# Optimization experiments

Hardware: AMD Instinct MI355X
Metric: run time of the kernel (lower is better)

The kernel has to match this reference:

```python
import jax, jax.numpy as jnp
import numpy as np

N_NODES = 100000
N_EDGES = 3200000
D_IN = 128
D_OUT = 128


def setup_inputs() -> dict:
    key = jax.random.key(0)
    k1, k2, k3, k4, k5, k6 = jax.random.split(key, 6)
    x = jax.random.normal(k1, (N_NODES, D_IN), dtype=jnp.float32)
    edge_row = jax.random.randint(k2, (N_EDGES,), 0, N_NODES)  # destination (adj row)
    edge_col = jax.random.randint(k3, (N_EDGES,), 0, N_NODES)  # source (adj col)
    edge_vals = jax.random.uniform(k4, (N_EDGES,), dtype=jnp.float32)
    stdv = 1.0 / np.sqrt(D_OUT)
    weight = jax.random.uniform(k5, (D_IN, D_OUT), dtype=jnp.float32, minval=-stdv, maxval=stdv)
    bias_param = jax.random.uniform(k6, (D_OUT,), dtype=jnp.float32, minval=-stdv, maxval=stdv)
    return {"x": x, "edge_row": edge_row, "edge_col": edge_col,
            "edge_vals": edge_vals, "weight": weight, "bias_param": bias_param}


def reference(x, edge_row, edge_col, edge_vals, weight, bias_param):
    # support = X @ W  : [N, D_OUT]
    support = x @ weight
    # output = spmm(adj, support): out[r] += v * support[c] for each edge (r, c, v)
    messages = edge_vals[:, None] * support[edge_col]  # [E, D_OUT]
    output = jax.ops.segment_sum(messages, edge_row, num_segments=N_NODES)
    return output + bias_param
```

## Files before the change

### kernel.cpp

```cpp
#include <hip/hip_runtime.h>

typedef unsigned int u32;
typedef unsigned long long u64;
typedef unsigned short u16;
typedef unsigned char u8;

#define NN 100000
#define NE 3200000
#define DIM 128
#define RB 256
#define NBK 391
#define BCAP 9216
#define EB 4096

#define OFF_OFFS 0
#define OFF_WB 400064
#define OFF_BCUR 432832
#define OFF_CVP 434432
#define OFF_SH 13234432
#define SCV_BYTES 14417664

typedef __attribute__((ext_vector_type(8))) short bf16x8;
typedef __attribute__((ext_vector_type(4))) float f32x4;

__device__ __forceinline__ float bflo(u32 b) { return __uint_as_float(b << 16); }
__device__ __forceinline__ float bfhi(u32 b) { return __uint_as_float(b & 0xffff0000u); }
__device__ __forceinline__ u16 f2bf(float f) {
    u32 u = __float_as_uint(f);
    return (u16)((u + 0x7fffu + ((u >> 16) & 1u)) >> 16);
}

__global__ __launch_bounds__(256) void bin_kernel(const int4* __restrict__ erow4,
                                                  const int4* __restrict__ ecol4,
                                                  const float4* __restrict__ ev4,
                                                  int* __restrict__ bcur,
                                                  u32* __restrict__ scv,
                                                  u8* __restrict__ slr,
                                                  const float* __restrict__ wf,
                                                  uint4* __restrict__ wB4) {
    __shared__ u32 sscv[EB];
    __shared__ u32 skey[EB];
    __shared__ int sa[512], sb[512], rs[512];
    __shared__ int base[NBK], lcur[NBK];
    int t = threadIdx.x;
    int gid = blockIdx.x * 256 + t;
    if (gid < 2048) {
        int tile = gid >> 6, l = gid & 63;
        int kt = tile >> 3, n = tile & 7;
        int col = n * 16 + (l & 15);
        int kb = kt * 32 + (l >> 4) * 8;
        u32 wp[4];
#pragma unroll
        for (int jj = 0; jj < 4; ++jj) {
            float w0 = wf[(kb + 2 * jj) * DIM + col];
            float w1 = wf[(kb + 2 * jj + 1) * DIM + col];
            wp[jj] = (u32)f2bf(w0) | ((u32)f2bf(w1) << 16);
        }
        wB4[tile * 64 + l] = make_uint4(wp[0], wp[1], wp[2], wp[3]);
    }
    int e0 = blockIdx.x * EB;
    int nval = min(EB, NE - e0);
    int4 er[4];
    bool val[4];
#pragma unroll
    for (int k = 0; k < 4; ++k) {
        int idx4 = (e0 >> 2) + k * 256 + t;
        val[k] = idx4 < NE / 4;
        er[k] = val[k] ? erow4[idx4] : make_int4(0, 0, 0, 0);
    }
    for (int i = t; i < 512; i += 256) sa[i] = 0;
    __syncthreads();
#pragma unroll
    for (int k = 0; k < 4; ++k) {
        if (val[k]) {
            atomicAdd(&sa[er[k].x >> 8], 1);
            atomicAdd(&sa[er[k].y >> 8], 1);
            atomicAdd(&sa[er[k].z >> 8], 1);
            atomicAdd(&sa[er[k].w >> 8], 1);
        }
    }
    __syncthreads();
    for (int i = t; i < NBK; i += 256) base[i] = atomicAdd(&bcur[i], sa[i]);
    int* pa = sa; int* pb = sb;
    for (int d = 1; d < 512; d <<= 1) {
        for (int i = t; i < 512; i += 256)
            pb[i] = (i >= d) ? (pa[i] + pa[i - d]) : pa[i];
        __syncthreads();
        int* tmp = pa; pa = pb; pb = tmp;
    }
    for (int i = t; i < 512; i += 256) {
        int ex = i ? pa[i - 1] : 0;
        rs[i] = ex;
        if (i < NBK) lcur[i] = ex;
    }
    __syncthreads();
#pragma unroll
    for (int k = 0; k < 4; ++k) {
        if (val[k]) {
            int idx4 = (e0 >> 2) + k * 256 + t;
            int4 c = ecol4[idx4];
            float4 v = ev4[idx4];
            int r, b, pos;
            r = er[k].x; b = r >> 8; pos = atomicAdd(&lcur[b], 1);
            sscv[pos] = ((u32)f2bf(v.x) << 17) | (u32)c.x; skey[pos] = ((u32)b << 8) | (u32)(r & 255);
            r = er[k].y; b = r >> 8; pos = atomicAdd(&lcur[b], 1);
            sscv[pos] = ((u32)f2bf(v.y) << 17) | (u32)c.y; skey[pos] = ((u32)b << 8) | (u32)(r & 255);
            r = er[k].z; b = r >> 8; pos = atomicAdd(&lcur[b], 1);
            sscv[pos] = ((u32)f2bf(v.z) << 17) | (u32)c.z; skey[pos] = ((u32)b << 8) | (u32)(r & 255);
            r = er[k].w; b = r >> 8; pos = atomicAdd(&lcur[b], 1);
            sscv[pos] = ((u32)f2bf(v.w) << 17) | (u32)c.w; skey[pos] = ((u32)b << 8) | (u32)(r & 255);
        }
    }
    __syncthreads();
    for (int i = t; i < nval; i += 256) {
        u32 key = skey[i];
        int bk = key >> 8;
        int gl = base[bk] + (i - rs[bk]);
        if (gl < BCAP) {
            scv[bk * BCAP + gl] = sscv[i];
            slr[bk * BCAP + gl] = (u8)(key & 255);
        }
    }
}

__global__ __launch_bounds__(256) void csr_kernel(const u32* __restrict__ scv,
                                                  const u8* __restrict__ slr,
                                                  const int* __restrict__ bcur,
                                                  int* __restrict__ offs,
                                                  u32* __restrict__ cvp) {
    __shared__ u32 lcv[BCAP];
    __shared__ int sa[RB], sb[RB], lcur[RB], red[256];
    int b = blockIdx.x, t = threadIdx.x;
    int r0 = b * RB;
    int rows = min(RB, NN - r0);
    int n = min(bcur[b], BCAP);
    int p = 0;
    for (int i = t; i < b; i += 256) p += min(bcur[i], BCAP);
    red[t] = p;
    sa[t] = 0;
    __syncthreads();
    for (int d = 128; d; d >>= 1) {
        if (t < d) red[t] += red[t + d];
        __syncthreads();
    }
    int gbase = red[0];
    if (b == NBK - 1 && t == 0) offs[NN] = gbase + n;
    const u32* scvB = scv + (size_t)b * BCAP;
    const u8* slrB = slr + (size_t)b * BCAP;
    for (int i = t; i < n; i += 256) atomicAdd(&sa[slrB[i]], 1);
    __syncthreads();
    int* pa = sa; int* pb = sb;
    for (int d = 1; d < 256; d <<= 1) {
        pb[t] = (t >= d) ? (pa[t] + pa[t - d]) : pa[t];
        __syncthreads();
        int* tmp = pa; pa = pb; pb = tmp;
    }
    int excl = t ? pa[t - 1] : 0;
    if (t < rows) offs[r0 + t] = gbase + excl;
    lcur[t] = excl;
    __syncthreads();
    for (int i = t; i < n; i += 256) {
        u32 cv = scvB[i];
        int lr = slrB[i];
        int pos = atomicAdd(&lcur[lr], 1);
        lcv[pos] = cv;
    }
    __syncthreads();
    for (int i = t; i < n; i += 256) cvp[gbase + i] = lcv[i];
}

__global__ __launch_bounds__(256) void gemm_kernel(const float4* __restrict__ xf4,
                                                   const uint4* __restrict__ wB4,
                                                   u32* __restrict__ sup) {
    __shared__ u32 st[64][68];
    int t = threadIdx.x, wave = t >> 6, lane = t & 63;
    int l15 = lane & 15, kg = lane >> 4;
    int row = blockIdx.x * 64 + wave * 16 + l15;
    int rc = min(row, NN - 1);
    f32x4 acc[8];
#pragma unroll
    for (int n = 0; n < 8; ++n) acc[n] = (f32x4){0.f, 0.f, 0.f, 0.f};
#pragma unroll
    for (int kt = 0; kt < 4; ++kt) {
        int k0 = kt * 32 + kg * 8;
        int bidx = (rc * DIM + k0) >> 2;
        float4 xa = xf4[bidx];
        float4 xc = xf4[bidx + 1];
        union { u32 u[4]; bf16x8 v; } A;
        A.u[0] = (u32)f2bf(xa.x) | ((u32)f2bf(xa.y) << 16);
        A.u[1] = (u32)f2bf(xa.z) | ((u32)f2bf(xa.w) << 16);
        A.u[2] = (u32)f2bf(xc.x) | ((u32)f2bf(xc.y) << 16);
        A.u[3] = (u32)f2bf(xc.z) | ((u32)f2bf(xc.w) << 16);
#pragma unroll
        for (int n = 0; n < 8; ++n) {
            union { uint4 u; bf16x8 v; } B;
            B.u = wB4[(kt * 8 + n) * 64 + lane];
            acc[n] = __builtin_amdgcn_mfma_f32_16x16x32_bf16(A.v, B.v, acc[n], 0, 0, 0);
        }
    }
    u16* stp = (u16*)st;
    int rbase = wave * 16 + kg * 4;
#pragma unroll
    for (int n = 0; n < 8; ++n)
#pragma unroll
        for (int i = 0; i < 4; ++i)
            stp[(rbase + i) * 136 + n * 16 + l15] = f2bf(acc[n][i]);
    __syncthreads();
    int r0 = blockIdx.x * 64;
    int rmax = min(64, NN - r0);
    for (int idx = t; idx < 4096; idx += 256) {
        int r = idx >> 6, c = idx & 63;
        if (r < rmax) sup[(r0 + r) * 64 + c] = st[r][c];
    }
}

template <int Q>
__device__ __forceinline__ void gstep(u32 pv, int kk, const u32* __restrict__ sup,
                                      int lane, float& a0, float& a1) {
    u32 ps[Q], xr[Q];
#pragma unroll
    for (int q = 0; q < Q; ++q)
        ps[q] = (u32)__builtin_amdgcn_readlane((int)pv, kk + q);
#pragma unroll
    for (int q = 0; q < Q; ++q)
        xr[q] = __hip_atomic_load(sup + ((ps[q] & 0x1ffffu) << 6) + lane,
                                  __ATOMIC_RELAXED, __HIP_MEMORY_SCOPE_AGENT);
#pragma unroll
    for (int q = 0; q < Q; ++q) {
        float v = bflo(ps[q] >> 17);
        a0 = fmaf(v, bflo(xr[q]), a0);
        a1 = fmaf(v, bfhi(xr[q]), a1);
    }
}

__global__ __launch_bounds__(64) void fused_kernel(const int* __restrict__ offs,
                                                   const u32* __restrict__ cvp,
                                                   const u32* __restrict__ sup,
                                                   const float2* __restrict__ bf2v,
                                                   u64* __restrict__ out) {
    int lane = threadIdx.x;
    int gw = blockIdx.x;
    int start = offs[gw];
    int end = offs[gw + 1];
    int cnt = end - start;
    float2 bp = bf2v[lane];
    float a0 = bp.x, a1 = bp.y;
    for (int j = 0; j < cnt; j += 64) {
        u32 pv = (j + lane < cnt) ? __builtin_nontemporal_load(&cvp[start + j + lane]) : 0u;
        int rem = min(64, cnt - j);
        int kk = 0;
        for (; kk + 32 <= rem; kk += 32) gstep<32>(pv, kk, sup, lane, a0, a1);
        for (; kk < rem; kk += 8) gstep<8>(pv, kk, sup, lane, a0, a1);
    }
    u64 bits = (u64)__float_as_uint(a0) | ((u64)__float_as_uint(a1) << 32);
    __builtin_nontemporal_store(bits, &out[gw * 64 + lane]);
}

extern "C" void kernel_launch(void* const* d_in, const int* in_sizes, int n_in,
                              void* d_out, int out_size, void* d_ws, size_t ws_size,
                              hipStream_t stream) {
    const float* x = (const float*)d_in[0];
    const int* erow = (const int*)d_in[1];
    const int* ecol = (const int*)d_in[2];
    const float* ev = (const float*)d_in[3];
    const float* wf = (const float*)d_in[4];
    const float2* bf2v = (const float2*)d_in[5];

    char* ws = (char*)d_ws;
    int* offs = (int*)(ws + OFF_OFFS);
    uint4* wB4 = (uint4*)(ws + OFF_WB);
    int* bcur = (int*)(ws + OFF_BCUR);
    u32* cvp = (u32*)(ws + OFF_CVP);
    u32* scv = (u32*)(ws + OFF_SH);
    u8* slr = (u8*)(ws + OFF_SH + SCV_BYTES);
    u32* sup = (u32*)(ws + OFF_SH);

    hipMemsetAsync(bcur, 0, NBK * sizeof(int), stream);

    bin_kernel<<<(NE + EB - 1) / EB, 256, 0, stream>>>((const int4*)erow, (const int4*)ecol,
                                                       (const float4*)ev, bcur,
                                                       scv, slr, wf, wB4);
    csr_kernel<<<NBK, 256, 0, stream>>>(scv, slr, bcur, offs, cvp);
    gemm_kernel<<<(NN + 63) / 64, 256, 0, stream>>>((const float4*)x, wB4, sup);
    fused_kernel<<<NN, 64, 0, stream>>>(offs, cvp, sup, bf2v, (u64*)d_out);
}
```

Before: 309.1 us.

## Double binning edges per block, vectorize CSR reads, pack two rows per SpMM block

Result: faster. 282.6 us (-8.6%).

```diff
diff --git a/kernel.cpp b/kernel.cpp
--- a/kernel.cpp
+++ b/kernel.cpp
@@ -11,7 +11,7 @@
 #define RB 256
 #define NBK 391
 #define BCAP 9216
-#define EB 4096
+#define EB 8192
 
 #define OFF_OFFS 0
 #define OFF_WB 400064
@@ -60,10 +60,10 @@
     }
     int e0 = blockIdx.x * EB;
     int nval = min(EB, NE - e0);
-    int4 er[4];
-    bool val[4];
-#pragma unroll
-    for (int k = 0; k < 4; ++k) {
+    int4 er[8];
+    bool val[8];
+#pragma unroll
+    for (int k = 0; k < 8; ++k) {
         int idx4 = (e0 >> 2) + k * 256 + t;
         val[k] = idx4 < NE / 4;
         er[k] = val[k] ? erow4[idx4] : make_int4(0, 0, 0, 0);
@@ -71,7 +71,7 @@
     for (int i = t; i < 512; i += 256) sa[i] = 0;
     __syncthreads();
 #pragma unroll
-    for (int k = 0; k < 4; ++k) {
+    for (int k = 0; k < 8; ++k) {
         if (val[k]) {
             atomicAdd(&sa[er[k].x >> 8], 1);
             atomicAdd(&sa[er[k].y >> 8], 1);
@@ -95,7 +95,7 @@
     }
     __syncthreads();
 #pragma unroll
-    for (int k = 0; k < 4; ++k) {
+    for (int k = 0; k < 8; ++k) {
         if (val[k]) {
             int idx4 = (e0 >> 2) + k * 256 + t;
             int4 c = ecol4[idx4];
@@ -147,7 +147,17 @@
     if (b == NBK - 1 && t == 0) offs[NN] = gbase + n;
     const u32* scvB = scv + (size_t)b * BCAP;
     const u8* slrB = slr + (size_t)b * BCAP;
-    for (int i = t; i < n; i += 256) atomicAdd(&sa[slrB[i]], 1);
+    const u32* slr4 = (const u32*)slrB;
+    const uint4* scv4 = (const uint4*)scvB;
+    int n4 = n >> 2;
+    for (int i = t; i < n4; i += 256) {
+        u32 w = slr4[i];
+        atomicAdd(&sa[w & 255], 1);
+        atomicAdd(&sa[(w >> 8) & 255], 1);
+        atomicAdd(&sa[(w >> 16) & 255], 1);
+        atomicAdd(&sa[w >> 24], 1);
+    }
+    for (int i = (n4 << 2) + t; i < n; i += 256) atomicAdd(&sa[slrB[i]], 1);
     __syncthreads();
     int* pa = sa; int* pb = sb;
     for (int d = 1; d < 256; d <<= 1) {
@@ -159,11 +169,18 @@
     if (t < rows) offs[r0 + t] = gbase + excl;
     lcur[t] = excl;
     __syncthreads();
-    for (int i = t; i < n; i += 256) {
-        u32 cv = scvB[i];
-        int lr = slrB[i];
-        int pos = atomicAdd(&lcur[lr], 1);
-        lcv[pos] = cv;
+    for (int i = t; i < n4; i += 256) {
+        uint4 cvq = scv4[i];
+        u32 w = slr4[i];
+        int pos;
+        pos = atomicAdd(&lcur[w & 255], 1);         lcv[pos] = cvq.x;
+        pos = atomicAdd(&lcur[(w >> 8) & 255], 1);  lcv[pos] = cvq.y;
+        pos = atomicAdd(&lcur[(w >> 16) & 255], 1); lcv[pos] = cvq.z;
+        pos = atomicAdd(&lcur[w >> 24], 1);         lcv[pos] = cvq.w;
+    }
+    for (int i = (n4 << 2) + t; i < n; i += 256) {
+        int pos = atomicAdd(&lcur[slrB[i]], 1);
+        lcv[pos] = scvB[i];
     }
     __syncthreads();
     for (int i = t; i < n; i += 256) cvp[gbase + i] = lcv[i];
@@ -233,13 +250,14 @@
     }
 }
 
-__global__ __launch_bounds__(64) void fused_kernel(const int* __restrict__ offs,
-                                                   const u32* __restrict__ cvp,
-                                                   const u32* __restrict__ sup,
-                                                   const float2* __restrict__ bf2v,
-                                                   u64* __restrict__ out) {
-    int lane = threadIdx.x;
-    int gw = blockIdx.x;
+__global__ __launch_bounds__(128) void fused_kernel(const int* __restrict__ offs,
+                                                    const u32* __restrict__ cvp,
+                                                    const u32* __restrict__ sup,
+                                                    const float2* __restrict__ bf2v,
+                                                    u64* __restrict__ out) {
+    int t = threadIdx.x;
+    int wave = t >> 6, lane = t & 63;
+    int gw = blockIdx.x * 2 + wave;
     int start = offs[gw];
     int end = offs[gw + 1];
     int cnt = end - start;
@@ -253,7 +271,7 @@
         for (; kk < rem; kk += 8) gstep<8>(pv, kk, sup, lane, a0, a1);
     }
     u64 bits = (u64)__float_as_uint(a0) | ((u64)__float_as_uint(a1) << 32);
-    __builtin_nontemporal_store(bits, &out[gw * 64 + lane]);
+    __builtin_nontemporal_store(bits, &out[(size_t)gw * 64 + lane]);
 }
 
 extern "C" void kernel_launch(void* const* d_in, const int* in_sizes, int n_in,
@@ -282,5 +300,5 @@
                                                        scv, slr, wf, wB4);
     csr_kernel<<<NBK, 256, 0, stream>>>(scv, slr, bcur, offs, cvp);
     gemm_kernel<<<(NN + 63) / 64, 256, 0, stream>>>((const float4*)x, wB4, sup);
-    fused_kernel<<<NN, 64, 0, stream>>>(offs, cvp, sup, bf2v, (u64*)d_out);
-}
+    fused_kernel<<<NN / 2, 128, 0, stream>>>(offs, cvp, sup, bf2v, (u64*)d_out);
+}
```
